# Kernel tuning notes

Measured on AMD Instinct MI355X. Metric: run time of the kernel, lower is better.

## Reference

```python
import jax, jax.numpy as jnp
import numpy as np

B, T, D_IN, N_UNITS, N_OUT = 128, 2048, 256, 512, 64
EPS, GAMMA = 0.01, 0.01


def setup_inputs() -> dict:
    key = jax.random.key(0)
    ks = jax.random.split(key, 5)
    x = jax.random.normal(ks[0], (B, T, D_IN), dtype=jnp.float32)
    # Linear weights ~ N(0, 1/input_dim) per the torch init
    Vh_w = jax.random.normal(ks[1], (N_UNITS, D_IN), dtype=jnp.float32) / D_IN
    Vh_b = jnp.zeros((N_UNITS,), dtype=jnp.float32)
    Vz_w = jax.random.normal(ks[2], (N_UNITS, D_IN), dtype=jnp.float32) / D_IN
    Vz_b = jnp.zeros((N_UNITS,), dtype=jnp.float32)
    # W ~ N(0, init_W_std/input_dim), square [n_units, n_units]
    W = jax.random.normal(ks[3], (N_UNITS, N_UNITS), dtype=jnp.float32) / D_IN
    fc_w = jax.random.normal(ks[4], (N_OUT, N_UNITS), dtype=jnp.float32) * 0.02
    fc_b = jnp.zeros((N_OUT,), dtype=jnp.float32)
    return {"x": x, "Vh_w": Vh_w, "Vh_b": Vh_b, "Vz_w": Vz_w, "Vz_b": Vz_b,
            "W": W, "fc_w": fc_w, "fc_b": fc_b}


def reference(x, Vh_w, Vh_b, Vz_w, Vz_b, W, fc_w, fc_b):
    n_units = W.shape[0]
    # precompute antisymmetric-minus-diffusion matrix once
    A = W - W.T - GAMMA * jnp.eye(n_units, dtype=W.dtype)
    # precompute input projections for all timesteps (batched GEMM)
    vh_x = jnp.einsum('btd,nd->btn', x, Vh_w) + Vh_b  # [B,T,N]
    vz_x = jnp.einsum('btd,nd->btn', x, Vz_w) + Vz_b  # [B,T,N]

    def step(h, inp):
        vh_t, vz_t = inp
        WmWT_h = h @ A                       # [B,N]
        f = jnp.tanh(WmWT_h + vh_t) * jax.nn.sigmoid(WmWT_h + vz_t)
        h = h + EPS * f
        return h, None

    h0 = jnp.zeros((x.shape[0], n_units), dtype=x.dtype)
    # scan over time: inputs shaped [T,B,N]
    hT, _ = jax.lax.scan(step, h0,
                         (jnp.swapaxes(vh_x, 0, 1), jnp.swapaxes(vz_x, 0, 1)))
    return hT @ fc_w.T + fc_b
```

## Files before the change

kernel.cpp:

```cpp
#include <hip/hip_runtime.h>
#include <stdint.h>

#define B_SZ   128
#define T_LEN  2048
#define DIN    256
#define NU     512
#define NOUT   64
#define EPS_F  0.01f
#define GAM_F  0.01f
#define KT     32
#define NTILES (T_LEN / KT)

typedef uint32_t u32;
typedef _Float16 h16;
typedef _Float16 __attribute__((ext_vector_type(2))) h16x2;
typedef _Float16 __attribute__((ext_vector_type(8))) h16x8;
typedef float    __attribute__((ext_vector_type(4))) f32x4;
typedef unsigned int __attribute__((ext_vector_type(4))) u32x4;

#define WS_A    0
#define WS_WH   131072
#define WS_WZ   196608
#define WS_EXCH 262144
#define NQUAD   43

__device__ __forceinline__ u32 pack2(float lo, float hi) {
  h16x2 v; v.x = (h16)lo; v.y = (h16)hi;
  return __builtin_bit_cast(u32, v);
}

__device__ __forceinline__ float fdot2(u32 h2, u32 a2, float acc) {
#if __has_builtin(__builtin_amdgcn_fdot2)
  return __builtin_amdgcn_fdot2(__builtin_bit_cast(h16x2, h2),
                                __builtin_bit_cast(h16x2, a2), acc, false);
#else
  h16x2 hh = __builtin_bit_cast(h16x2, h2);
  h16x2 aa = __builtin_bit_cast(h16x2, a2);
  return acc + (float)hh.x * (float)aa.x + (float)hh.y * (float)aa.y;
#endif
}

__global__ void antirnn_prep(const float* __restrict__ Vh_w,
                             const float* __restrict__ Vz_w,
                             const float* __restrict__ W,
                             u32* __restrict__ ws,
                             float* __restrict__ out) {
  const int idx = blockIdx.x * blockDim.x + threadIdx.x;
  const int stride = gridDim.x * blockDim.x;

  for (int u = idx; u < 131072; u += stride) {
    int e  = u & 3;
    int l  = (u >> 2) & 63;
    int pq = (u >> 8) & 15;
    int c4 = (u >> 12) & 3;
    int w  = (u >> 14) & 3;
    int jh = (u >> 16) & 1;
    int p  = pq * 4 + e;
    int i0 = w * 128 + 2 * p;
    int j  = jh * 256 + l * 4 + c4;
    float lo = W[i0 * NU + j]       - W[j * NU + i0]     - (i0 == j     ? GAM_F : 0.f);
    float hi = W[(i0 + 1) * NU + j] - W[j * NU + i0 + 1] - ((i0 + 1) == j ? GAM_F : 0.f);
    ws[WS_A + u] = pack2(lo, hi);
  }
  for (int u = idx; u < 65536; u += stride) {
    int fl = u * 2;
    ws[WS_WH + u] = pack2(Vh_w[fl], Vh_w[fl + 1]);
    ws[WS_WZ + u] = pack2(Vz_w[fl], Vz_w[fl + 1]);
  }
  for (int u = idx; u < B_SZ * 2 * 2 * NQUAD * 4; u += stride) ws[WS_EXCH + u] = 0;
  for (int u = idx; u < B_SZ * NOUT; u += stride) out[u] = 0.f;
}

__global__ __launch_bounds__(256, 1) void antirnn_scan(
    const float* __restrict__ x,
    const float* __restrict__ vh_b, const float* __restrict__ vz_b,
    const float* __restrict__ fc_w, const float* __restrict__ fc_b,
    u32* __restrict__ ws, float* __restrict__ out) {

  __shared__ h16  xs[32 * 256];
  __shared__ h16  ph[256 * 36];
  __shared__ h16  pz[256 * 36];
  __shared__ float part[4 * 256];
  __shared__ u32  hp[256];

  const int tid = threadIdx.x;
  const int w   = tid >> 6;
  const int l   = tid & 63;
  const int bid = blockIdx.x;
  const int b   = bid & 127;
  const int jh  = bid >> 7;

  u32 a[256];
  {
    const uint4* Ap = reinterpret_cast<const uint4*>(ws + WS_A) + (jh * 4 + w) * 4096 + l;
#pragma unroll
    for (int rq = 0; rq < 64; ++rq) {
      uint4 q = Ap[rq * 64];
      int base = (rq >> 4) * 64 + (rq & 15) * 4;
      a[base + 0] = q.x; a[base + 1] = q.y; a[base + 2] = q.z; a[base + 3] = q.w;
    }
  }

  hp[tid] = 0;

  const float* xrow = x + (long)b * T_LEN * DIN;
  float hreg = 0.f;
  const h16* Wn_h = reinterpret_cast<const h16*>(ws + WS_WH);
  const h16* Wn_z = reinterpret_cast<const h16*>(ws + WS_WZ);
  uint4* exch = reinterpret_cast<uint4*>(ws + WS_EXCH);

  const int  peerHalf   = 1 - jh;
  const bool isPeerWave = ((w >> 1) == peerHalf);
  const int  qbase      = (w & 1) * 21;

#pragma unroll 1
  for (int tile = 0; tile < NTILES; ++tile) {
#pragma unroll
    for (int it = 0; it < 16; ++it) {
      int fp = it * 256 + tid;
      int s  = fp >> 7, dp = fp & 127;
      float2 v = *reinterpret_cast<const float2*>(xrow + (tile * KT + s) * DIN + dp * 2);
      int byteaddr = (s * 512 + dp * 4) ^ ((s & 7) << 4);
      *reinterpret_cast<u32*>(reinterpret_cast<char*>(xs) + byteaddr) = pack2(v.x, v.y);
    }
    __syncthreads();

    {
      f32x4 acch[2][4], accz[2][4];
#pragma unroll
      for (int mt = 0; mt < 2; ++mt)
#pragma unroll
        for (int nt = 0; nt < 4; ++nt) {
          acch[mt][nt] = (f32x4){0.f, 0.f, 0.f, 0.f};
          accz[mt][nt] = (f32x4){0.f, 0.f, 0.f, 0.f};
        }
      const int lk = (l >> 4) * 8;
      const int ln = l & 15;
#pragma unroll
      for (int kk = 0; kk < 8; ++kk) {
        h16x8 af[2];
#pragma unroll
        for (int mt = 0; mt < 2; ++mt) {
          int s = mt * 16 + ln;
          int byteaddr = (s * 512 + kk * 64 + (l >> 4) * 16) ^ ((s & 7) << 4);
          af[mt] = *reinterpret_cast<const h16x8*>(reinterpret_cast<const char*>(xs) + byteaddr);
        }
#pragma unroll
        for (int nt = 0; nt < 4; ++nt) {
          int ng = jh * 256 + w * 64 + nt * 16 + ln;
          h16x8 bh = *reinterpret_cast<const h16x8*>(Wn_h + ng * 256 + kk * 32 + lk);
          h16x8 bz = *reinterpret_cast<const h16x8*>(Wn_z + ng * 256 + kk * 32 + lk);
#pragma unroll
          for (int mt = 0; mt < 2; ++mt) {
            acch[mt][nt] = __builtin_amdgcn_mfma_f32_16x16x32_f16(af[mt], bh, acch[mt][nt], 0, 0, 0);
            accz[mt][nt] = __builtin_amdgcn_mfma_f32_16x16x32_f16(af[mt], bz, accz[mt][nt], 0, 0, 0);
          }
        }
      }
#pragma unroll
      for (int nt = 0; nt < 4; ++nt) {
        int n  = w * 64 + nt * 16 + ln;
        float bh_ = vh_b[jh * 256 + n];
        float bz_ = vz_b[jh * 256 + n];
#pragma unroll
        for (int mt = 0; mt < 2; ++mt) {
          int s0 = mt * 16 + (l >> 4) * 4;
          *reinterpret_cast<u32*>(&ph[n * 36 + s0])     = pack2(acch[mt][nt].x + bh_, acch[mt][nt].y + bh_);
          *reinterpret_cast<u32*>(&ph[n * 36 + s0 + 2]) = pack2(acch[mt][nt].z + bh_, acch[mt][nt].w + bh_);
          *reinterpret_cast<u32*>(&pz[n * 36 + s0])     = pack2(accz[mt][nt].x + bz_, accz[mt][nt].y + bz_);
          *reinterpret_cast<u32*>(&pz[n * 36 + s0 + 2]) = pack2(accz[mt][nt].z + bz_, accz[mt][nt].w + bz_);
        }
      }
    }
    __syncthreads();

#pragma unroll 1
    for (int s = 0; s < KT; ++s) {
      const int t = tile * KT + s;

      if (isPeerWave && t > 0 && l <= 21) {
        int q = qbase + l;
        const uint4* src = exch + (((b * 2 + peerHalf) * 2 + (t & 1)) * NQUAD) + q;
        u32x4 v;
        do {
          asm volatile("global_load_dwordx4 %0, %1, off sc0 sc1\n\ts_waitcnt vmcnt(0)"
                       : "=v"(v) : "v"(src) : "memory");
        } while (v[0] != (u32)t);
#pragma unroll
        for (int k2 = 0; k2 < 3; ++k2) {
          int pi = q * 3 + k2;
          if (pi < 128) hp[peerHalf * 128 + pi] = v[1 + k2];
        }
      }

      u32 hq[64];
      {
        const uint4* hpw = reinterpret_cast<const uint4*>(&hp[w * 64]);
#pragma unroll
        for (int pq = 0; pq < 16; ++pq) {
          uint4 qq = hpw[pq];
          hq[pq * 4 + 0] = qq.x; hq[pq * 4 + 1] = qq.y;
          hq[pq * 4 + 2] = qq.z; hq[pq * 4 + 3] = qq.w;
        }
      }
      float acc0 = 0.f, acc1 = 0.f, acc2 = 0.f, acc3 = 0.f;
#pragma unroll
      for (int p = 0; p < 64; ++p) {
        acc0 = fdot2(hq[p], a[p],        acc0);
        acc1 = fdot2(hq[p], a[64 + p],   acc1);
        acc2 = fdot2(hq[p], a[128 + p],  acc2);
        acc3 = fdot2(hq[p], a[192 + p],  acc3);
      }
      {
        f32x4 pv = {acc0, acc1, acc2, acc3};
        *reinterpret_cast<f32x4*>(&part[w * 256 + l * 4]) = pv;
      }
      __syncthreads();

      {
        float pre = part[tid] + part[256 + tid] + part[512 + tid] + part[768 + tid];
        float uh  = pre + (float)ph[tid * 36 + s];
        float uz  = pre + (float)pz[tid * 36 + s];
        float uhc = fminf(fmaxf(uh, -20.f), 20.f);
        float e2  = __expf(2.f * uhc);
        float th  = 1.f - 2.f / (e2 + 1.f);
        float sg  = 1.f / (1.f + __expf(-uz));
        hreg += EPS_F * th * sg;
        float other = __shfl_xor(hreg, 1, 64);
        if (!(tid & 1)) hp[jh * 128 + (tid >> 1)] = pack2(hreg, other);
      }
      __syncthreads();

      if ((t + 1 < T_LEN) && w == 0 && l < NQUAD) {
        int p0 = l * 3;
        u32 v0 = hp[jh * 128 + p0];
        u32 v1 = (p0 + 1 < 128) ? hp[jh * 128 + p0 + 1] : 0u;
        u32 v2 = (p0 + 2 < 128) ? hp[jh * 128 + p0 + 2] : 0u;
        u32x4 qd; qd[0] = (u32)(t + 1); qd[1] = v0; qd[2] = v1; qd[3] = v2;
        uint4* dst = exch + (((b * 2 + jh) * 2 + ((t + 1) & 1)) * NQUAD) + l;
        asm volatile("global_store_dwordx4 %0, %1, off sc0 sc1"
                     :: "v"(dst), "v"(qd) : "memory");
      }
    }
  }

  __syncthreads();
  part[tid] = hreg;
  __syncthreads();
  if (tid < NOUT) {
    float acc = (jh == 0) ? fc_b[tid] : 0.f;
    const float* fr = fc_w + tid * NU + jh * 256;
#pragma unroll 4
    for (int c = 0; c < 256; ++c) acc += part[c] * fr[c];
    atomicAdd(out + b * NOUT + tid, acc);
  }
}

extern "C" void kernel_launch(void* const* d_in, const int* in_sizes, int n_in,
                              void* d_out, int out_size, void* d_ws, size_t ws_size,
                              hipStream_t stream) {
  const float* x    = (const float*)d_in[0];
  const float* Vh_w = (const float*)d_in[1];
  const float* Vh_b = (const float*)d_in[2];
  const float* Vz_w = (const float*)d_in[3];
  const float* Vz_b = (const float*)d_in[4];
  const float* W    = (const float*)d_in[5];
  const float* fc_w = (const float*)d_in[6];
  const float* fc_b = (const float*)d_in[7];
  float* out = (float*)d_out;
  u32*   ws  = (u32*)d_ws;

  antirnn_prep<<<512, 256, 0, stream>>>(Vh_w, Vz_w, W, ws, out);
  antirnn_scan<<<256, 256, 0, stream>>>(x, Vh_b, Vz_b, fc_w, fc_b, ws, out);
}
```

Measured before the change: 4.993 ms.

## Run each batch row in one 512-thread block with MFMA recurrence and overlapped projection

The split of each batch row across two blocks is removed, along with the per-step global-memory spin exchange of half the hidden state. One 512-thread block now owns a whole batch row and needs only one block barrier per timestep. The recurrent matvec becomes MFMA with the antisymmetric matrix split between registers and LDS (filled via global_load_lds). The input projection for the next tile is computed piecewise between recurrence steps so its loads and MFMAs overlap the serial chain. The costs are half as many blocks on the device, redundant MFMA rows (the hidden vector is broadcast across all 16 rows), and one wasted projection of a wrapped tile at the end.

Result: slower. 7.098 ms (+42.1%).

```diff
diff --git a/kernel.cpp b/kernel.cpp
--- a/kernel.cpp
+++ b/kernel.cpp
@@ -8,7 +8,7 @@
 #define NOUT   64
 #define EPS_F  0.01f
 #define GAM_F  0.01f
-#define KT     32
+#define KT     16
 #define NTILES (T_LEN / KT)
 
 typedef uint32_t u32;
@@ -16,243 +16,238 @@
 typedef _Float16 __attribute__((ext_vector_type(2))) h16x2;
 typedef _Float16 __attribute__((ext_vector_type(8))) h16x8;
 typedef float    __attribute__((ext_vector_type(4))) f32x4;
-typedef unsigned int __attribute__((ext_vector_type(4))) u32x4;
-
-#define WS_A    0
-#define WS_WH   131072
-#define WS_WZ   196608
-#define WS_EXCH 262144
-#define NQUAD   43
+
+typedef const __attribute__((address_space(1))) u32* gas_u32p;
+typedef __attribute__((address_space(3))) u32* las_u32p;
+
+#define WS_A  0
+#define WS_WH 131072
+#define WS_WZ 196608
 
 __device__ __forceinline__ u32 pack2(float lo, float hi) {
   h16x2 v; v.x = (h16)lo; v.y = (h16)hi;
   return __builtin_bit_cast(u32, v);
 }
-
-__device__ __forceinline__ float fdot2(u32 h2, u32 a2, float acc) {
-#if __has_builtin(__builtin_amdgcn_fdot2)
-  return __builtin_amdgcn_fdot2(__builtin_bit_cast(h16x2, h2),
-                                __builtin_bit_cast(h16x2, a2), acc, false);
-#else
-  h16x2 hh = __builtin_bit_cast(h16x2, h2);
-  h16x2 aa = __builtin_bit_cast(h16x2, a2);
-  return acc + (float)hh.x * (float)aa.x + (float)hh.y * (float)aa.y;
-#endif
-}
+__device__ __forceinline__ h16x8 as8(uint4 q) { return __builtin_bit_cast(h16x8, q); }
 
 __global__ void antirnn_prep(const float* __restrict__ Vh_w,
                              const float* __restrict__ Vz_w,
                              const float* __restrict__ W,
-                             u32* __restrict__ ws,
-                             float* __restrict__ out) {
+                             u32* __restrict__ ws) {
   const int idx = blockIdx.x * blockDim.x + threadIdx.x;
   const int stride = gridDim.x * blockDim.x;
 
   for (int u = idx; u < 131072; u += stride) {
     int e  = u & 3;
     int l  = (u >> 2) & 63;
-    int pq = (u >> 8) & 15;
-    int c4 = (u >> 12) & 3;
-    int w  = (u >> 14) & 3;
-    int jh = (u >> 16) & 1;
-    int p  = pq * 4 + e;
-    int i0 = w * 128 + 2 * p;
-    int j  = jh * 256 + l * 4 + c4;
-    float lo = W[i0 * NU + j]       - W[j * NU + i0]     - (i0 == j     ? GAM_F : 0.f);
-    float hi = W[(i0 + 1) * NU + j] - W[j * NU + i0 + 1] - ((i0 + 1) == j ? GAM_F : 0.f);
+    int q  = (u >> 8) & 63;
+    int w  = (u >> 14) & 7;
+    int nt = q >> 4, kk = q & 15;
+    int j  = w * 64 + nt * 16 + (l & 15);
+    int k0 = kk * 32 + (l >> 4) * 8 + 2 * e;
+    int k1 = k0 + 1;
+    float lo = W[k0 * NU + j] - W[j * NU + k0] - (k0 == j ? GAM_F : 0.f);
+    float hi = W[k1 * NU + j] - W[j * NU + k1] - (k1 == j ? GAM_F : 0.f);
     ws[WS_A + u] = pack2(lo, hi);
   }
   for (int u = idx; u < 65536; u += stride) {
-    int fl = u * 2;
-    ws[WS_WH + u] = pack2(Vh_w[fl], Vh_w[fl + 1]);
-    ws[WS_WZ + u] = pack2(Vz_w[fl], Vz_w[fl + 1]);
-  }
-  for (int u = idx; u < B_SZ * 2 * 2 * NQUAD * 4; u += stride) ws[WS_EXCH + u] = 0;
-  for (int u = idx; u < B_SZ * NOUT; u += stride) out[u] = 0.f;
-}
-
-__global__ __launch_bounds__(256, 1) void antirnn_scan(
+    int e  = u & 3;
+    int l  = (u >> 2) & 63;
+    int q2 = (u >> 8) & 31;
+    int w  = (u >> 13) & 7;
+    int nt = q2 >> 3, kk = q2 & 7;
+    int n  = w * 64 + nt * 16 + (l & 15);
+    int k0 = kk * 32 + (l >> 4) * 8 + 2 * e;
+    ws[WS_WH + u] = pack2(Vh_w[n * DIN + k0], Vh_w[n * DIN + k0 + 1]);
+    ws[WS_WZ + u] = pack2(Vz_w[n * DIN + k0], Vz_w[n * DIN + k0 + 1]);
+  }
+}
+
+__global__ __launch_bounds__(512, 2) void antirnn_scan(
     const float* __restrict__ x,
     const float* __restrict__ vh_b, const float* __restrict__ vz_b,
     const float* __restrict__ fc_w, const float* __restrict__ fc_b,
-    u32* __restrict__ ws, float* __restrict__ out) {
-
-  __shared__ h16  xs[32 * 256];
-  __shared__ h16  ph[256 * 36];
-  __shared__ h16  pz[256 * 36];
-  __shared__ float part[4 * 256];
-  __shared__ u32  hp[256];
+    const u32* __restrict__ ws, float* __restrict__ out) {
+
+  __shared__ u32 ldsA[15 * 8 * 64 * 4];
+  __shared__ u32 phz[2 * 8 * 512];
+  __shared__ u32 hp[2][256];
 
   const int tid = threadIdx.x;
   const int w   = tid >> 6;
   const int l   = tid & 63;
-  const int bid = blockIdx.x;
-  const int b   = bid & 127;
-  const int jh  = bid >> 7;
-
-  u32 a[256];
-  {
-    const uint4* Ap = reinterpret_cast<const uint4*>(ws + WS_A) + (jh * 4 + w) * 4096 + l;
-#pragma unroll
-    for (int rq = 0; rq < 64; ++rq) {
-      uint4 q = Ap[rq * 64];
-      int base = (rq >> 4) * 64 + (rq & 15) * 4;
-      a[base + 0] = q.x; a[base + 1] = q.y; a[base + 2] = q.z; a[base + 3] = q.w;
-    }
-  }
-
-  hp[tid] = 0;
-
-  const float* xrow = x + (long)b * T_LEN * DIN;
-  float hreg = 0.f;
-  const h16* Wn_h = reinterpret_cast<const h16*>(ws + WS_WH);
-  const h16* Wn_z = reinterpret_cast<const h16*>(ws + WS_WZ);
-  uint4* exch = reinterpret_cast<uint4*>(ws + WS_EXCH);
-
-  const int  peerHalf   = 1 - jh;
-  const bool isPeerWave = ((w >> 1) == peerHalf);
-  const int  qbase      = (w & 1) * 21;
+  const int lg  = l >> 4;
+  const int ln  = l & 15;
+  const int col = tid;
+  const int b   = blockIdx.x;
+
+  uint4 areg[49];
+  const uint4* wsA4 = reinterpret_cast<const uint4*>(ws + WS_A);
+#pragma unroll
+  for (int nt = 0; nt < 4; ++nt)
+#pragma unroll
+    for (int kk = 0; kk < 16; ++kk) {
+      const int RC = (nt == 0) ? 13 : 12;
+      if (kk < RC) {
+        const int slot = (nt == 0) ? kk : 13 + (nt - 1) * 12 + kk;
+        areg[slot] = wsA4[(w * 64 + nt * 16 + kk) * 64 + l];
+      }
+    }
+#pragma unroll
+  for (int nt = 0; nt < 4; ++nt)
+#pragma unroll
+    for (int kk = 0; kk < 16; ++kk) {
+      const int RC = (nt == 0) ? 13 : 12;
+      if (kk >= RC) {
+        const int ls = (nt == 0) ? (kk - 13) : 3 + (nt - 1) * 4 + (kk - 12);
+        const u32* src = ws + WS_A + ((w * 64 + nt * 16 + kk) * 64 + l) * 4;
+        __builtin_amdgcn_global_load_lds((gas_u32p)src,
+                                         (las_u32p)&ldsA[(w * 15 + ls) * 256], 16, 0, 0);
+      }
+    }
+
+  if (tid < 256) { hp[0][tid] = 0; hp[1][tid] = 0; }
+  const float bh = vh_b[col], bz = vz_b[col];
+  float hval = 0.f;
+
+  const uint4* wsWH4 = reinterpret_cast<const uint4*>(ws + WS_WH);
+  const uint4* wsWZ4 = reinterpret_cast<const uint4*>(ws + WS_WZ);
+  const float* xb = x + (long)b * T_LEN * DIN;
+  u32 stash[16];
+
+  asm volatile("s_waitcnt vmcnt(0)" ::: "memory");
+  __syncthreads();
+
+#pragma unroll
+  for (int p = 0; p < 4; ++p) {
+    const uint4* wsW = (p >> 1) ? wsWZ4 : wsWH4;
+    const int ntA = (p & 1) * 2, ntB = ntA + 1;
+    f32x4 pacc0 = {0.f, 0.f, 0.f, 0.f}, pacc1 = {0.f, 0.f, 0.f, 0.f};
+#pragma unroll 1
+    for (int kkp = 0; kkp < 8; ++kkp) {
+      const float* xr = xb + (long)ln * DIN + kkp * 32 + lg * 8;
+      float4 x0 = *reinterpret_cast<const float4*>(xr);
+      float4 x1 = *reinterpret_cast<const float4*>(xr + 4);
+      h16x8 xf;
+      xf[0]=(h16)x0.x; xf[1]=(h16)x0.y; xf[2]=(h16)x0.z; xf[3]=(h16)x0.w;
+      xf[4]=(h16)x1.x; xf[5]=(h16)x1.y; xf[6]=(h16)x1.z; xf[7]=(h16)x1.w;
+      h16x8 wf0 = as8(wsW[(w * 32 + ntA * 8 + kkp) * 64 + l]);
+      h16x8 wf1 = as8(wsW[(w * 32 + ntB * 8 + kkp) * 64 + l]);
+      pacc0 = __builtin_amdgcn_mfma_f32_16x16x32_f16(xf, wf0, pacc0, 0, 0, 0);
+      pacc1 = __builtin_amdgcn_mfma_f32_16x16x32_f16(xf, wf1, pacc1, 0, 0, 0);
+    }
+    stash[p*4+0] = pack2(pacc0.x, pacc0.y); stash[p*4+1] = pack2(pacc0.z, pacc0.w);
+    stash[p*4+2] = pack2(pacc1.x, pacc1.y); stash[p*4+3] = pack2(pacc1.z, pacc1.w);
+  }
+#pragma unroll
+  for (int p = 0; p < 4; ++p) {
+    const int arr = p >> 1;
+#pragma unroll
+    for (int ntx = 0; ntx < 2; ++ntx) {
+      const int nt = (p & 1) * 2 + ntx;
+      const int cb = w * 64 + nt * 16 + ln;
+      phz[(arr * 8 + lg * 2 + 0) * 512 + cb] = stash[p*4 + ntx*2 + 0];
+      phz[(arr * 8 + lg * 2 + 1) * 512 + cb] = stash[p*4 + ntx*2 + 1];
+    }
+  }
+  __syncthreads();
 
 #pragma unroll 1
   for (int tile = 0; tile < NTILES; ++tile) {
-#pragma unroll
-    for (int it = 0; it < 16; ++it) {
-      int fp = it * 256 + tid;
-      int s  = fp >> 7, dp = fp & 127;
-      float2 v = *reinterpret_cast<const float2*>(xrow + (tile * KT + s) * DIN + dp * 2);
-      int byteaddr = (s * 512 + dp * 4) ^ ((s & 7) << 4);
-      *reinterpret_cast<u32*>(reinterpret_cast<char*>(xs) + byteaddr) = pack2(v.x, v.y);
-    }
-    __syncthreads();
-
-    {
-      f32x4 acch[2][4], accz[2][4];
-#pragma unroll
-      for (int mt = 0; mt < 2; ++mt)
-#pragma unroll
-        for (int nt = 0; nt < 4; ++nt) {
-          acch[mt][nt] = (f32x4){0.f, 0.f, 0.f, 0.f};
-          accz[mt][nt] = (f32x4){0.f, 0.f, 0.f, 0.f};
+    const int tsrc = (tile + 1) & (NTILES - 1);
+    const float* xtb = xb + (long)tsrc * KT * DIN;
+
+#pragma unroll
+    for (int p = 0; p < 4; ++p) {
+      const uint4* wsW = (p >> 1) ? wsWZ4 : wsWH4;
+      const int ntA = (p & 1) * 2, ntB = ntA + 1;
+      f32x4 pacc0 = {0.f, 0.f, 0.f, 0.f}, pacc1 = {0.f, 0.f, 0.f, 0.f};
+
+#pragma unroll 1
+      for (int sp = 0; sp < 4; ++sp) {
+#pragma unroll
+        for (int kh = 0; kh < 2; ++kh) {
+          const int kkp = sp * 2 + kh;
+          const float* xr = xtb + (long)ln * DIN + kkp * 32 + lg * 8;
+          float4 x0 = *reinterpret_cast<const float4*>(xr);
+          float4 x1 = *reinterpret_cast<const float4*>(xr + 4);
+          h16x8 xf;
+          xf[0]=(h16)x0.x; xf[1]=(h16)x0.y; xf[2]=(h16)x0.z; xf[3]=(h16)x0.w;
+          xf[4]=(h16)x1.x; xf[5]=(h16)x1.y; xf[6]=(h16)x1.z; xf[7]=(h16)x1.w;
+          h16x8 wf0 = as8(wsW[(w * 32 + ntA * 8 + kkp) * 64 + l]);
+          h16x8 wf1 = as8(wsW[(w * 32 + ntB * 8 + kkp) * 64 + l]);
+          pacc0 = __builtin_amdgcn_mfma_f32_16x16x32_f16(xf, wf0, pacc0, 0, 0, 0);
+          pacc1 = __builtin_amdgcn_mfma_f32_16x16x32_f16(xf, wf1, pacc1, 0, 0, 0);
         }
-      const int lk = (l >> 4) * 8;
-      const int ln = l & 15;
-#pragma unroll
-      for (int kk = 0; kk < 8; ++kk) {
-        h16x8 af[2];
-#pragma unroll
-        for (int mt = 0; mt < 2; ++mt) {
-          int s = mt * 16 + ln;
-          int byteaddr = (s * 512 + kk * 64 + (l >> 4) * 16) ^ ((s & 7) << 4);
-          af[mt] = *reinterpret_cast<const h16x8*>(reinterpret_cast<const char*>(xs) + byteaddr);
+
+        const u32* hpc = hp[sp & 1];
+        u32* hpn = hp[1 - (sp & 1)];
+        f32x4 a0 = {0.f,0.f,0.f,0.f}, a1 = a0, a2 = a0, a3 = a0;
+#pragma unroll
+        for (int kk = 0; kk < 16; ++kk) {
+          h16x8 hf = *reinterpret_cast<const h16x8*>(hpc + kk * 16 + lg * 4);
+          h16x8 b0, b1, b2, b3;
+          if (kk < 13) b0 = as8(areg[kk]);
+          else         b0 = *reinterpret_cast<const h16x8*>(&ldsA[(w*15 + (kk-13)) * 256 + l * 4]);
+          if (kk < 12) b1 = as8(areg[13 + kk]);
+          else         b1 = *reinterpret_cast<const h16x8*>(&ldsA[(w*15 + 3 + (kk-12)) * 256 + l * 4]);
+          if (kk < 12) b2 = as8(areg[25 + kk]);
+          else         b2 = *reinterpret_cast<const h16x8*>(&ldsA[(w*15 + 7 + (kk-12)) * 256 + l * 4]);
+          if (kk < 12) b3 = as8(areg[37 + kk]);
+          else         b3 = *reinterpret_cast<const h16x8*>(&ldsA[(w*15 + 11 + (kk-12)) * 256 + l * 4]);
+          a0 = __builtin_amdgcn_mfma_f32_16x16x32_f16(hf, b0, a0, 0, 0, 0);
+          a1 = __builtin_amdgcn_mfma_f32_16x16x32_f16(hf, b1, a1, 0, 0, 0);
+          a2 = __builtin_amdgcn_mfma_f32_16x16x32_f16(hf, b2, a2, 0, 0, 0);
+          a3 = __builtin_amdgcn_mfma_f32_16x16x32_f16(hf, b3, a3, 0, 0, 0);
         }
-#pragma unroll
-        for (int nt = 0; nt < 4; ++nt) {
-          int ng = jh * 256 + w * 64 + nt * 16 + ln;
-          h16x8 bh = *reinterpret_cast<const h16x8*>(Wn_h + ng * 256 + kk * 32 + lk);
-          h16x8 bz = *reinterpret_cast<const h16x8*>(Wn_z + ng * 256 + kk * 32 + lk);
-#pragma unroll
-          for (int mt = 0; mt < 2; ++mt) {
-            acch[mt][nt] = __builtin_amdgcn_mfma_f32_16x16x32_f16(af[mt], bh, acch[mt][nt], 0, 0, 0);
-            accz[mt][nt] = __builtin_amdgcn_mfma_f32_16x16x32_f16(af[mt], bz, accz[mt][nt], 0, 0, 0);
-          }
+
+        {
+          const int s2 = p * 2 + (sp >> 1);
+          float pre = (lg == 0) ? a0.x : (lg == 1) ? a1.x : (lg == 2) ? a2.x : a3.x;
+          h16x2 ph2 = __builtin_bit_cast(h16x2, phz[s2 * 512 + col]);
+          h16x2 pz2 = __builtin_bit_cast(h16x2, phz[(8 + s2) * 512 + col]);
+          float vh = (float)ph2[sp & 1];
+          float vz = (float)pz2[sp & 1];
+          float uh = pre + vh + bh;
+          float uz = pre + vz + bz;
+          float uhc = fminf(fmaxf(uh, -20.f), 20.f);
+          float e2  = __expf(2.f * uhc);
+          float th  = 1.f - 2.f / (e2 + 1.f);
+          float sg  = 1.f / (1.f + __expf(-uz));
+          hval += EPS_F * th * sg;
+          float oth = __shfl_xor(hval, 1, 64);
+          if (!(col & 1)) hpn[col >> 1] = pack2(hval, oth);
         }
-      }
-#pragma unroll
-      for (int nt = 0; nt < 4; ++nt) {
-        int n  = w * 64 + nt * 16 + ln;
-        float bh_ = vh_b[jh * 256 + n];
-        float bz_ = vz_b[jh * 256 + n];
-#pragma unroll
-        for (int mt = 0; mt < 2; ++mt) {
-          int s0 = mt * 16 + (l >> 4) * 4;
-          *reinterpret_cast<u32*>(&ph[n * 36 + s0])     = pack2(acch[mt][nt].x + bh_, acch[mt][nt].y + bh_);
-          *reinterpret_cast<u32*>(&ph[n * 36 + s0 + 2]) = pack2(acch[mt][nt].z + bh_, acch[mt][nt].w + bh_);
-          *reinterpret_cast<u32*>(&pz[n * 36 + s0])     = pack2(accz[mt][nt].x + bz_, accz[mt][nt].y + bz_);
-          *reinterpret_cast<u32*>(&pz[n * 36 + s0 + 2]) = pack2(accz[mt][nt].z + bz_, accz[mt][nt].w + bz_);
-        }
-      }
-    }
-    __syncthreads();
-
-#pragma unroll 1
-    for (int s = 0; s < KT; ++s) {
-      const int t = tile * KT + s;
-
-      if (isPeerWave && t > 0 && l <= 21) {
-        int q = qbase + l;
-        const uint4* src = exch + (((b * 2 + peerHalf) * 2 + (t & 1)) * NQUAD) + q;
-        u32x4 v;
-        do {
-          asm volatile("global_load_dwordx4 %0, %1, off sc0 sc1\n\ts_waitcnt vmcnt(0)"
-                       : "=v"(v) : "v"(src) : "memory");
-        } while (v[0] != (u32)t);
-#pragma unroll
-        for (int k2 = 0; k2 < 3; ++k2) {
-          int pi = q * 3 + k2;
-          if (pi < 128) hp[peerHalf * 128 + pi] = v[1 + k2];
-        }
-      }
-
-      u32 hq[64];
-      {
-        const uint4* hpw = reinterpret_cast<const uint4*>(&hp[w * 64]);
-#pragma unroll
-        for (int pq = 0; pq < 16; ++pq) {
-          uint4 qq = hpw[pq];
-          hq[pq * 4 + 0] = qq.x; hq[pq * 4 + 1] = qq.y;
-          hq[pq * 4 + 2] = qq.z; hq[pq * 4 + 3] = qq.w;
-        }
-      }
-      float acc0 = 0.f, acc1 = 0.f, acc2 = 0.f, acc3 = 0.f;
-#pragma unroll
-      for (int p = 0; p < 64; ++p) {
-        acc0 = fdot2(hq[p], a[p],        acc0);
-        acc1 = fdot2(hq[p], a[64 + p],   acc1);
-        acc2 = fdot2(hq[p], a[128 + p],  acc2);
-        acc3 = fdot2(hq[p], a[192 + p],  acc3);
-      }
-      {
-        f32x4 pv = {acc0, acc1, acc2, acc3};
-        *reinterpret_cast<f32x4*>(&part[w * 256 + l * 4]) = pv;
-      }
-      __syncthreads();
-
-      {
-        float pre = part[tid] + part[256 + tid] + part[512 + tid] + part[768 + tid];
-        float uh  = pre + (float)ph[tid * 36 + s];
-        float uz  = pre + (float)pz[tid * 36 + s];
-        float uhc = fminf(fmaxf(uh, -20.f), 20.f);
-        float e2  = __expf(2.f * uhc);
-        float th  = 1.f - 2.f / (e2 + 1.f);
-        float sg  = 1.f / (1.f + __expf(-uz));
-        hreg += EPS_F * th * sg;
-        float other = __shfl_xor(hreg, 1, 64);
-        if (!(tid & 1)) hp[jh * 128 + (tid >> 1)] = pack2(hreg, other);
-      }
-      __syncthreads();
-
-      if ((t + 1 < T_LEN) && w == 0 && l < NQUAD) {
-        int p0 = l * 3;
-        u32 v0 = hp[jh * 128 + p0];
-        u32 v1 = (p0 + 1 < 128) ? hp[jh * 128 + p0 + 1] : 0u;
-        u32 v2 = (p0 + 2 < 128) ? hp[jh * 128 + p0 + 2] : 0u;
-        u32x4 qd; qd[0] = (u32)(t + 1); qd[1] = v0; qd[2] = v1; qd[3] = v2;
-        uint4* dst = exch + (((b * 2 + jh) * 2 + ((t + 1) & 1)) * NQUAD) + l;
-        asm volatile("global_store_dwordx4 %0, %1, off sc0 sc1"
-                     :: "v"(dst), "v"(qd) : "memory");
-      }
-    }
-  }
-
-  __syncthreads();
-  part[tid] = hreg;
+        __syncthreads();
+      }
+
+      stash[p*4+0] = pack2(pacc0.x, pacc0.y); stash[p*4+1] = pack2(pacc0.z, pacc0.w);
+      stash[p*4+2] = pack2(pacc1.x, pacc1.y); stash[p*4+3] = pack2(pacc1.z, pacc1.w);
+    }
+
+#pragma unroll
+    for (int p = 0; p < 4; ++p) {
+      const int arr = p >> 1;
+#pragma unroll
+      for (int ntx = 0; ntx < 2; ++ntx) {
+        const int nt = (p & 1) * 2 + ntx;
+        const int cb = w * 64 + nt * 16 + ln;
+        phz[(arr * 8 + lg * 2 + 0) * 512 + cb] = stash[p*4 + ntx*2 + 0];
+        phz[(arr * 8 + lg * 2 + 1) * 512 + cb] = stash[p*4 + ntx*2 + 1];
+      }
+    }
+  }
+
+  __syncthreads();
+  float* hbuf = reinterpret_cast<float*>(phz);
+  hbuf[col] = hval;
   __syncthreads();
   if (tid < NOUT) {
-    float acc = (jh == 0) ? fc_b[tid] : 0.f;
-    const float* fr = fc_w + tid * NU + jh * 256;
+    float acc = fc_b[tid];
+    const float* fr = fc_w + tid * NU;
 #pragma unroll 4
-    for (int c = 0; c < 256; ++c) acc += part[c] * fr[c];
-    atomicAdd(out + b * NOUT + tid, acc);
+    for (int c = 0; c < NU; ++c) acc += hbuf[c] * fr[c];
+    out[b * NOUT + tid] = acc;
   }
 }
 
@@ -270,6 +265,6 @@
   float* out = (float*)d_out;
   u32*   ws  = (u32*)d_ws;
 
-  antirnn_prep<<<512, 256, 0, stream>>>(Vh_w, Vz_w, W, ws, out);
-  antirnn_scan<<<256, 256, 0, stream>>>(x, Vh_b, Vz_b, fc_w, fc_b, ws, out);
-}
+  antirnn_prep<<<512, 256, 0, stream>>>(Vh_w, Vz_w, W, ws);
+  antirnn_scan<<<128, 512, 0, stream>>>(x, Vh_b, Vz_b, fc_w, fc_b, ws, out);
+}
```
